# Kernel optimization log

Hardware: AMD Instinct MI355X
Metric: run time of the kernel (lower is better)

The kernel has to match this reference:

```python
import jax, jax.numpy as jnp
import numpy as np

BOS = 1
MAX_LEN = 20


def _lstm_cell(x, h, c, Wih, Whh, bih, bhh):
    # torch.nn.LSTMCell gate order: i, f, g, o
    g = x @ Wih.T + h @ Whh.T + bih + bhh
    i, f, gg, o = jnp.split(g, 4, axis=-1)
    c = jax.nn.sigmoid(f) * c + jax.nn.sigmoid(i) * jnp.tanh(gg)
    h = jax.nn.sigmoid(o) * jnp.tanh(c)
    return h, c


def setup_inputs() -> dict:
    key = jax.random.key(0)
    ks = jax.random.split(key, 12)
    B, K, D = 512, 36, 2048
    A, H, Em, V = 512, 512, 300, 10000
    s = 0.02
    rn = lambda k, shape, sc=s: sc * jax.random.normal(k, shape, dtype=jnp.float32)
    return {
        'feats': jax.random.normal(ks[0], (B, K, D), dtype=jnp.float32),
        'Wp': rn(ks[1], (A, D)), 'bp': jnp.zeros((A,), jnp.float32),
        'E': rn(ks[2], (V, Em), 0.1).at[0].set(0.0),  # padding_idx = 0
        'Wih1': rn(ks[3], (4 * H, Em + A)), 'Whh1': rn(ks[4], (4 * H, H)),
        'bih1': jnp.zeros((4 * H,), jnp.float32), 'bhh1': jnp.zeros((4 * H,), jnp.float32),
        'Wih2': rn(ks[5], (4 * H, H + A)), 'Whh2': rn(ks[6], (4 * H, H)),
        'bih2': jnp.zeros((4 * H,), jnp.float32), 'bhh2': jnp.zeros((4 * H,), jnp.float32),
        'Wa1': rn(ks[7], (A, H + A)), 'ba1': jnp.zeros((A,), jnp.float32),
        'wa2': rn(ks[8], (1, A)), 'ba2': jnp.zeros((1,), jnp.float32),
        'Wo': rn(ks[9], (V, H)), 'bo': jnp.zeros((V,), jnp.float32),
    }


def reference(feats, Wp, bp, E, Wih1, Whh1, bih1, bhh1, Wih2, Whh2, bih2, bhh2,
              Wa1, ba1, wa2, ba2, Wo, bo):
    B, K, D = feats.shape
    H = Whh1.shape[1]
    f_att = feats @ Wp.T + bp                      # [B, K, A]
    f_mean = f_att.mean(axis=1)                    # [B, A]
    # attn Linear over concat([h1, f_att]): split columns, precompute f_att term
    Wa1_h, Wa1_f = Wa1[:, :H], Wa1[:, H:]
    att_f = f_att @ Wa1_f.T + ba1                  # [B, K, A]
    x0 = jnp.broadcast_to(E[BOS], (B, E.shape[1]))
    z = jnp.zeros((B, H), jnp.float32)
    carry0 = (x0, z, z, z, z)

    def step(carry, _):
        x, h1, c1, h2, c2 = carry
        h1, c1 = _lstm_cell(jnp.concatenate([x, f_mean], axis=-1), h1, c1,
                            Wih1, Whh1, bih1, bhh1)
        pre = jnp.tanh(att_f + (h1 @ Wa1_h.T)[:, None, :])   # [B, K, A]
        e = pre @ wa2[0] + ba2[0]                            # [B, K]
        alpha = jax.nn.softmax(e, axis=-1)
        ctx = jnp.einsum('bk,bka->ba', alpha, f_att)         # [B, A]
        h2, c2 = _lstm_cell(jnp.concatenate([h1, ctx], axis=-1), h2, c2,
                            Wih2, Whh2, bih2, bhh2)
        logit = h2 @ Wo.T + bo                               # [B, V]  (dropout is identity in eval)
        nxt = jnp.argmax(logit, axis=-1)
        return (E[nxt], h1, c1, h2, c2), nxt

    _, ids = jax.lax.scan(step, carry0, None, length=MAX_LEN - 1)
    return ids.T  # [B, MAX_LEN-1], matches torch.stack(out_ids, 1)
```

## Files before the change

kernel.cpp:

```cpp
#include <hip/hip_runtime.h>
#include <math.h>
#include <stdint.h>

constexpr int Bsz = 512, Kf = 36, Dd = 2048, Aa = 512, Hh = 512, Em = 300;
constexpr int Vv = 10000, TSTEPS = 19, BOS = 1;
constexpr int K1 = 832;
constexpr int K2 = 1536;
constexpr int VvP = 10112;
constexpr float SPLIT_S  = 2048.0f;
constexpr float SPLIT_IS = 1.0f / 2048.0f;

#define CDIV(a,b) (((a)+(b)-1)/(b))

typedef _Float16 f16x8 __attribute__((ext_vector_type(8)));
typedef float    f32x4 __attribute__((ext_vector_type(4)));

typedef const unsigned int GU __attribute__((address_space(1)));
typedef unsigned int       LU __attribute__((address_space(3)));

__device__ __forceinline__ void gload16(const void* g, void* l) {
    __builtin_amdgcn_global_load_lds((GU*)g, (LU*)l, 16, 0, 0);
}

template<int N> __device__ __forceinline__ void wait_vm() {
    if constexpr (N == 0)       asm volatile("s_waitcnt vmcnt(0)" ::: "memory");
    else if constexpr (N == 4)  asm volatile("s_waitcnt vmcnt(4)" ::: "memory");
    else if constexpr (N == 6)  asm volatile("s_waitcnt vmcnt(6)" ::: "memory");
    else if constexpr (N == 8)  asm volatile("s_waitcnt vmcnt(8)" ::: "memory");
    else static_assert(N == 0, "unsupported vmcnt literal");
}
#define WAIT_LGKM asm volatile("s_waitcnt lgkmcnt(0)" ::: "memory")
#define SB0 __builtin_amdgcn_sched_barrier(0)
#define BAR __builtin_amdgcn_s_barrier()

__device__ __forceinline__ float sigm(float v) { return 1.0f / (1.0f + expf(-v)); }

__device__ __forceinline__ void wsplit(_Float16* __restrict__ hi, _Float16* __restrict__ lo,
                                       size_t idx, float v) {
    _Float16 h = (_Float16)v;
    hi[idx] = h;
    lo[idx] = (_Float16)((v - (float)h) * SPLIT_S);
}

template<int BM, int BN, int BK, bool AF32, bool NFAST, int OCC>
__global__ __launch_bounds__(256, OCC)
void gemm_sp(const float* __restrict__ Af,
             const _Float16* __restrict__ Ahi, const _Float16* __restrict__ Alo, int lda,
             const _Float16* __restrict__ Bhi, const _Float16* __restrict__ Blo, int ldb,
             float* __restrict__ C, int ldc, int N, int K,
             const float* __restrict__ bias1, const float* __restrict__ bias2,
             const float* __restrict__ addC, int gxn)
{
    constexpr int WM = BM / 2, WN = BN / 2;
    constexpr int MF = WM / 16, NF = WN / 16;
    constexpr int PA  = BK / 8;
    constexpr int PSA = BM * 8 + 8;
    constexpr int PSB = BN * 8 + 8;
    constexpr int SZA = PA * PSA, SZB = PA * PSB;
    constexpr int OAH = 0, OAL = SZA, OBH = 2 * SZA, OBL = 2 * SZA + SZB;
    constexpr int BUF = 2 * SZA + 2 * SZB;
    constexpr int NCHA = BM * BK / 2048;
    constexpr int NCHB = BN * BK / 2048;
    constexpr int LW = 2 * NCHA + 2 * NCHB;
    __shared__ _Float16 sm[2 * BUF];

    const int nwg = gridDim.x;
    const int cpx = nwg >> 3;
    const int orig = blockIdx.x;
    const int lid = (orig & 7) * cpx + (orig >> 3);
    int mt, nt;
    if (NFAST) { nt = lid % gxn; mt = lid / gxn; }
    else       { const int gym = nwg / gxn; mt = lid % gym; nt = lid / gym; }
    const int m0 = mt * BM, n0 = nt * BN;

    const int t    = threadIdx.x;
    const int lane = t & 63;
    const int w    = t >> 6;
    const int wr   = w >> 1, wc = w & 1;
    const int l15  = lane & 15, l4 = lane >> 4;

    f32x4 acch[MF][NF];
    f32x4 accm[MF][NF];
    #pragma unroll
    for (int m = 0; m < MF; ++m)
        #pragma unroll
        for (int n = 0; n < NF; ++n) {
            acch[m][n] = (f32x4){0.f, 0.f, 0.f, 0.f};
            accm[m][n] = (f32x4){0.f, 0.f, 0.f, 0.f};
        }

    const int nkt = K / BK;

    auto stageB = [&](int bufo, int kt) {
        #pragma unroll
        for (int i = 0; i < NCHB; ++i) {
            const int q  = i * 256 + t;
            const int p  = q / BN, r = q % BN;
            const int qw = i * 256 + (t & ~63);
            const int pu = qw / BN, ru = qw % BN;
            const size_t goff = (size_t)(n0 + r) * ldb + kt * BK + p * 8;
            gload16(Bhi + goff, &sm[bufo + OBH + pu * PSB + ru * 8]);
            gload16(Blo + goff, &sm[bufo + OBL + pu * PSB + ru * 8]);
        }
    };
    auto stageA16 = [&](int bufo, int kt) {
        #pragma unroll
        for (int i = 0; i < NCHA; ++i) {
            const int q  = i * 256 + t;
            const int p  = q / BM, r = q % BM;
            const int qw = i * 256 + (t & ~63);
            const int pu = qw / BM, ru = qw % BM;
            const size_t goff = (size_t)(m0 + r) * lda + kt * BK + p * 8;
            gload16(Ahi + goff, &sm[bufo + OAH + pu * PSA + ru * 8]);
            gload16(Alo + goff, &sm[bufo + OAL + pu * PSA + ru * 8]);
        }
    };
    auto issueA = [&](float4 (&rd)[NCHA][2], int kt) {
        #pragma unroll
        for (int i = 0; i < NCHA; ++i) {
            const int q = i * 256 + t;
            const int p = q / BM, r = q % BM;
            const float* src = Af + (size_t)(m0 + r) * lda + kt * BK + p * 8;
            rd[i][0] = *(const float4*)src;
            rd[i][1] = *(const float4*)(src + 4);
        }
    };
    auto writeA = [&](int bufo, float4 (&rd)[NCHA][2]) {
        #pragma unroll
        for (int i = 0; i < NCHA; ++i) {
            const int q = i * 256 + t;
            const int p = q / BM, r = q % BM;
            const float f[8] = {rd[i][0].x, rd[i][0].y, rd[i][0].z, rd[i][0].w,
                                rd[i][1].x, rd[i][1].y, rd[i][1].z, rd[i][1].w};
            f16x8 hi, lo;
            #pragma unroll
            for (int j = 0; j < 8; ++j) {
                _Float16 h = (_Float16)f[j];
                hi[j] = h;
                lo[j] = (_Float16)((f[j] - (float)h) * SPLIT_S);
            }
            *(f16x8*)&sm[bufo + OAH + p * PSA + r * 8] = hi;
            *(f16x8*)&sm[bufo + OAL + p * PSA + r * 8] = lo;
        }
    };
    auto compute = [&](int bufo) {
        #pragma unroll
        for (int s = 0; s < BK / 32; ++s) {
            f16x8 ah[MF], al[MF], bh[NF], bl[NF];
            const int pl = s * 4 + l4;
            #pragma unroll
            for (int m = 0; m < MF; ++m) {
                const int row = wr * WM + m * 16 + l15;
                ah[m] = *(const f16x8*)&sm[bufo + OAH + pl * PSA + row * 8];
                al[m] = *(const f16x8*)&sm[bufo + OAL + pl * PSA + row * 8];
            }
            #pragma unroll
            for (int n = 0; n < NF; ++n) {
                const int row = wc * WN + n * 16 + l15;
                bh[n] = *(const f16x8*)&sm[bufo + OBH + pl * PSB + row * 8];
                bl[n] = *(const f16x8*)&sm[bufo + OBL + pl * PSB + row * 8];
            }
            #pragma unroll
            for (int m = 0; m < MF; ++m)
                #pragma unroll
                for (int n = 0; n < NF; ++n) {
                    acch[m][n] = __builtin_amdgcn_mfma_f32_16x16x32_f16(ah[m], bh[n], acch[m][n], 0, 0, 0);
                    accm[m][n] = __builtin_amdgcn_mfma_f32_16x16x32_f16(ah[m], bl[n], accm[m][n], 0, 0, 0);
                    accm[m][n] = __builtin_amdgcn_mfma_f32_16x16x32_f16(al[m], bh[n], accm[m][n], 0, 0, 0);
                }
        }
    };

    if constexpr (AF32) {
        float4 rA[NCHA][2], rB[NCHA][2];
        issueA(rA, 0); stageB(0, 0);
        for (int kt = 0; kt < nkt; kt += 2) {
            issueA(rB, kt + 1); stageB(BUF, kt + 1);
            wait_vm<LW>(); SB0;
            writeA(0, rA);
            WAIT_LGKM; SB0;
            BAR; SB0;
            compute(0);
            SB0; WAIT_LGKM; BAR; SB0;
            if (kt + 2 < nkt) { issueA(rA, kt + 2); stageB(0, kt + 2); wait_vm<LW>(); }
            else              { wait_vm<0>(); }
            SB0;
            writeA(BUF, rB);
            WAIT_LGKM; SB0;
            BAR; SB0;
            compute(BUF);
            SB0; WAIT_LGKM; BAR; SB0;
        }
    } else {
        stageA16(0, 0); stageB(0, 0);
        for (int kt = 0; kt < nkt; ++kt) {
            const int bufc = (kt & 1) ? BUF : 0;
            const int bufn = BUF - bufc;
            if (kt + 1 < nkt) { stageA16(bufn, kt + 1); stageB(bufn, kt + 1); wait_vm<LW>(); }
            else              { wait_vm<0>(); }
            SB0;
            BAR; SB0;
            compute(bufc);
            SB0; WAIT_LGKM; BAR; SB0;
        }
    }

    #pragma unroll
    for (int m = 0; m < MF; ++m) {
        const int rowb = m0 + wr * WM + m * 16 + l4 * 4;
        #pragma unroll
        for (int n = 0; n < NF; ++n) {
            const int col = n0 + wc * WN + n * 16 + l15;
            if (col < N) {
                float bb = 0.f;
                if (bias1) bb += bias1[col];
                if (bias2) bb += bias2[col];
                #pragma unroll
                for (int r = 0; r < 4; ++r) {
                    const size_t idx = (size_t)(rowb + r) * ldc + col;
                    float v = acch[m][n][r] + accm[m][n][r] * SPLIT_IS + bb;
                    if (addC) v += addC[idx];
                    C[idx] = v;
                }
            }
        }
    }
}

__global__ __launch_bounds__(256)
void split_convert(const float* __restrict__ src, int srcld, int validR,
                   _Float16* __restrict__ dhi, _Float16* __restrict__ dlo,
                   int dstld, int coloff, int R, int C)
{
    const int total = R * C;
    for (int i = blockIdx.x * 256 + threadIdx.x; i < total; i += gridDim.x * 256) {
        const int r = i / C, c = i % C;
        const float v = (r < validR) ? src[(size_t)r * srcld + c] : 0.f;
        wsplit(dhi, dlo, (size_t)r * dstld + coloff + c, v);
    }
}

__global__ __launch_bounds__(256)
void transpose_wah(const float* __restrict__ Wa1, float* __restrict__ WahT)
{
    const int i = blockIdx.x * 256 + threadIdx.x;
    if (i < Aa * Hh) {
        const int a = i / Hh, h = i % Hh;
        WahT[(size_t)h * Aa + a] = Wa1[(size_t)a * (Hh + Aa) + h];
    }
}

__global__ __launch_bounds__(256)
void init_kernel(_Float16* __restrict__ a1h, _Float16* __restrict__ a1l,
                 _Float16* __restrict__ a2h, _Float16* __restrict__ a2l,
                 float* __restrict__ c1, float* __restrict__ c2,
                 const float* __restrict__ E)
{
    const int idx = blockIdx.x * 256 + threadIdx.x;
    if (idx < Bsz * K1) {
        const int col = idx % K1;
        const float v = (col < Em) ? E[(size_t)BOS * Em + col] : 0.f;
        wsplit(a1h, a1l, idx, v);
    }
    if (idx < Bsz * K2) wsplit(a2h, a2l, idx, 0.f);
    if (idx < Bsz * Hh) { c1[idx] = 0.f; c2[idx] = 0.f; }
}

__global__ __launch_bounds__(256)
void fmean_kernel(const float* __restrict__ f_att, float* __restrict__ f_mean,
                  _Float16* __restrict__ fmh, _Float16* __restrict__ fml)
{
    const int b = blockIdx.x;
    for (int a = threadIdx.x; a < Aa; a += 256) {
        float s = 0.f;
        for (int k = 0; k < Kf; ++k) s += f_att[((size_t)b * Kf + k) * Aa + a];
        const float v = s * (1.0f / 36.0f);
        f_mean[(size_t)b * Aa + a] = v;
        wsplit(fmh, fml, (size_t)b * Aa + a, v);
    }
}

__global__ __launch_bounds__(256)
void lstm_cell_kernel(const float* __restrict__ g, float* __restrict__ c,
                      _Float16* __restrict__ hhi, _Float16* __restrict__ hlo,
                      int hld, int hoff,
                      _Float16* __restrict__ h2hi, _Float16* __restrict__ h2lo,
                      int h2ld, int h2off)
{
    const int idx = blockIdx.x * 256 + threadIdx.x;
    const int b = idx >> 9, h = idx & 511;
    const float* gb = g + (size_t)b * 2048;
    const float gi = gb[h], gf = gb[512 + h], gc = gb[1024 + h], go = gb[1536 + h];
    const float cv = sigm(gf) * c[idx] + sigm(gi) * tanhf(gc);
    c[idx] = cv;
    const float hv = sigm(go) * tanhf(cv);
    wsplit(hhi, hlo, (size_t)b * hld + hoff + h, hv);
    if (h2hi) wsplit(h2hi, h2lo, (size_t)b * h2ld + h2off + h, hv);
}

__global__ __launch_bounds__(256)
void attn_fused(const float* __restrict__ att_f,
                const _Float16* __restrict__ a2hin, const _Float16* __restrict__ a2lin,
                const float* __restrict__ WahT,
                const float* __restrict__ wa2, const float* __restrict__ ba2,
                const float* __restrict__ f_att,
                _Float16* __restrict__ a2h, _Float16* __restrict__ a2l)
{
    const int b = blockIdx.x, tid = threadIdx.x;
    const int w = tid >> 6, lane = tid & 63;
    __shared__ float sh1[Hh];
    __shared__ float sq[Aa];
    __shared__ float se[Kf];
    __shared__ float wk[Kf];
    for (int h = tid; h < Hh; h += 256)
        sh1[h] = (float)a2hin[(size_t)b * K2 + h] + (float)a2lin[(size_t)b * K2 + h] * SPLIT_IS;
    __syncthreads();
    for (int a = tid; a < Aa; a += 256) {
        float acc = 0.f;
        for (int h = 0; h < Hh; ++h)
            acc = fmaf(sh1[h], WahT[(size_t)h * Aa + a], acc);
        sq[a] = acc;
    }
    __syncthreads();
    for (int k = w; k < Kf; k += 4) {
        const float* pf = att_f + ((size_t)b * Kf + k) * Aa;
        float s = 0.f;
        #pragma unroll
        for (int j = 0; j < Aa; j += 64) {
            const int a = j + lane;
            s += tanhf(pf[a] + sq[a]) * wa2[a];
        }
        #pragma unroll
        for (int off = 32; off; off >>= 1) s += __shfl_down(s, off);
        if (lane == 0) se[k] = s + ba2[0];
    }
    __syncthreads();
    if (tid < Kf) {
        float mx = -INFINITY;
        for (int k = 0; k < Kf; ++k) mx = fmaxf(mx, se[k]);
        float ssum = 0.f;
        for (int k = 0; k < Kf; ++k) ssum += expf(se[k] - mx);
        wk[tid] = expf(se[tid] - mx) / ssum;
    }
    __syncthreads();
    for (int a = tid; a < Aa; a += 256) {
        float acc = 0.f;
        for (int k = 0; k < Kf; ++k)
            acc = fmaf(wk[k], f_att[((size_t)b * Kf + k) * Aa + a], acc);
        wsplit(a2h, a2l, (size_t)b * K2 + Hh + a, acc);
    }
}

__global__ __launch_bounds__(256)
void argmax_embed_kernel(const float* __restrict__ logits, const float* __restrict__ E,
                         _Float16* __restrict__ a1h, _Float16* __restrict__ a1l,
                         int* __restrict__ out, int t)
{
    const int b = blockIdx.x;
    const int tid = threadIdx.x;
    float best = -INFINITY;
    int bi = Vv;
    for (int j = tid; j < Vv; j += 256) {
        const float v = logits[(size_t)b * Vv + j];
        if (v > best) { best = v; bi = j; }
    }
    __shared__ float sv[256];
    __shared__ int   si[256];
    sv[tid] = best; si[tid] = bi;
    __syncthreads();
    for (int s = 128; s > 0; s >>= 1) {
        if (tid < s) {
            const float v2 = sv[tid + s];
            const int   i2 = si[tid + s];
            if (v2 > sv[tid] || (v2 == sv[tid] && i2 < si[tid])) { sv[tid] = v2; si[tid] = i2; }
        }
        __syncthreads();
    }
    const int idx = si[0];
    if (tid == 0) out[(size_t)b * TSTEPS + t] = idx;
    for (int d = tid; d < Em; d += 256)
        wsplit(a1h, a1l, (size_t)b * K1 + d, E[(size_t)idx * Em + d]);
}

static inline void conv(hipStream_t s, const float* src, int srcld, int validR,
                        _Float16* dhi, _Float16* dlo, int dstld, int coloff, int R, int C)
{
    int blocks = CDIV(R * C, 256); if (blocks > 2048) blocks = 2048;
    split_convert<<<dim3(blocks), dim3(256), 0, s>>>(src, srcld, validR, dhi, dlo, dstld, coloff, R, C);
}

extern "C" void kernel_launch(void* const* d_in, const int* in_sizes, int n_in,
                              void* d_out, int out_size, void* d_ws, size_t ws_size,
                              hipStream_t stream)
{
    const float* feats = (const float*)d_in[0];
    const float* Wp    = (const float*)d_in[1];
    const float* bp    = (const float*)d_in[2];
    const float* E     = (const float*)d_in[3];
    const float* Wih1  = (const float*)d_in[4];
    const float* Whh1  = (const float*)d_in[5];
    const float* bih1  = (const float*)d_in[6];
    const float* bhh1  = (const float*)d_in[7];
    const float* Wih2  = (const float*)d_in[8];
    const float* Whh2  = (const float*)d_in[9];
    const float* bih2  = (const float*)d_in[10];
    const float* bhh2  = (const float*)d_in[11];
    const float* Wa1   = (const float*)d_in[12];
    const float* ba1   = (const float*)d_in[13];
    const float* wa2   = (const float*)d_in[14];
    const float* ba2   = (const float*)d_in[15];
    const float* Wo    = (const float*)d_in[16];
    const float* bo    = (const float*)d_in[17];
    int* out = (int*)d_out;
    (void)in_sizes; (void)n_in; (void)out_size; (void)ws_size;

    uint8_t* w = (uint8_t*)d_ws;
    size_t off = 0;
    auto alloc = [&](size_t bytes) { void* p = w + off; off = (off + bytes + 255) & ~(size_t)255; return p; };

    float*     f_att  = (float*)alloc(18432ull * 512 * 4);
    float*     att_f  = (float*)alloc(18432ull * 512 * 4);
    float*     f_mean = (float*)alloc(512ull * 512 * 4);
    _Float16*  fmh    = (_Float16*)alloc(512ull * 512 * 2);
    _Float16*  fml    = (_Float16*)alloc(512ull * 512 * 2);
    _Float16*  wph    = (_Float16*)alloc(512ull * 2048 * 2);
    _Float16*  wpl    = (_Float16*)alloc(512ull * 2048 * 2);
    _Float16*  w1ph   = (_Float16*)alloc(2048ull * K1 * 2);
    _Float16*  w1pl   = (_Float16*)alloc(2048ull * K1 * 2);
    _Float16*  w1ch   = (_Float16*)alloc(2048ull * 512 * 2);
    _Float16*  w1cl   = (_Float16*)alloc(2048ull * 512 * 2);
    _Float16*  w2ph   = (_Float16*)alloc(2048ull * K2 * 2);
    _Float16*  w2pl   = (_Float16*)alloc(2048ull * K2 * 2);
    float*     WahT   = (float*)alloc(512ull * 512 * 4);
    _Float16*  wafh   = (_Float16*)alloc(512ull * 512 * 2);
    _Float16*  wafl   = (_Float16*)alloc(512ull * 512 * 2);
    _Float16*  woh    = (_Float16*)alloc((size_t)VvP * 512 * 2);
    _Float16*  wol    = (_Float16*)alloc((size_t)VvP * 512 * 2);
    float*     g1c    = (float*)alloc(512ull * 2048 * 4);
    _Float16*  a1h    = (_Float16*)alloc(512ull * K1 * 2);
    _Float16*  a1l    = (_Float16*)alloc(512ull * K1 * 2);
    _Float16*  a2h    = (_Float16*)alloc(512ull * K2 * 2);
    _Float16*  a2l    = (_Float16*)alloc(512ull * K2 * 2);
    float*     c1     = (float*)alloc(512ull * 512 * 4);
    float*     c2     = (float*)alloc(512ull * 512 * 4);
    float*     gbuf   = (float*)alloc(512ull * 2048 * 4);
    float*     logits = (float*)alloc(512ull * Vv * 4);

    conv(stream, Wp,          Dd,      512,   wph,  wpl,  2048, 0,    512,  2048);
    conv(stream, Wih1,        Em + Aa, 2048,  w1ph, w1pl, K1,   0,    2048, Em);
    conv(stream, Whh1,        Hh,      2048,  w1ph, w1pl, K1,   Em,   2048, 512);
    conv(stream, Wih1,        Em + Aa, 0,     w1ph, w1pl, K1,   812,  2048, 20);
    conv(stream, Wih1 + Em,   Em + Aa, 2048,  w1ch, w1cl, 512,  0,    2048, 512);
    conv(stream, Wih2,        Hh + Aa, 2048,  w2ph, w2pl, K2,   0,    2048, 1024);
    conv(stream, Whh2,        Hh,      2048,  w2ph, w2pl, K2,   1024, 2048, 512);
    transpose_wah<<<dim3(1024), dim3(256), 0, stream>>>(Wa1, WahT);
    conv(stream, Wa1 + Hh,    Hh + Aa, 512,   wafh, wafl, 512,  0,    512,  512);
    conv(stream, Wo,          Hh,      Vv,    woh,  wol,  512,  0,    VvP,  512);

    init_kernel<<<dim3(CDIV(Bsz * K2, 256)), dim3(256), 0, stream>>>(a1h, a1l, a2h, a2l, c1, c2, E);

    gemm_sp<128, 64, 32, true, true, 2><<<dim3(1152), 256, 0, stream>>>(
        feats, nullptr, nullptr, Dd, wph, wpl, 2048, f_att, 512, 512, 2048, bp, nullptr, nullptr, 8);
    fmean_kernel<<<dim3(Bsz), dim3(256), 0, stream>>>(f_att, f_mean, fmh, fml);
    gemm_sp<64, 64, 32, false, false, 4><<<dim3(256), 256, 0, stream>>>(
        nullptr, fmh, fml, 512, w1ch, w1cl, 512, g1c, 2048, 2048, 512, bih1, bhh1, nullptr, 32);
    gemm_sp<128, 64, 32, true, true, 2><<<dim3(1152), 256, 0, stream>>>(
        f_att, nullptr, nullptr, 512, wafh, wafl, 512, att_f, 512, 512, 512, ba1, nullptr, nullptr, 8);

    for (int t = 0; t < TSTEPS; ++t) {
        gemm_sp<64, 64, 32, false, false, 4><<<dim3(256), 256, 0, stream>>>(
            nullptr, a1h, a1l, K1, w1ph, w1pl, K1, gbuf, 2048, 2048, K1, nullptr, nullptr, g1c, 32);
        lstm_cell_kernel<<<dim3(Bsz * Hh / 256), dim3(256), 0, stream>>>(
            gbuf, c1, a2h, a2l, K2, 0, a1h, a1l, K1, Em);
        attn_fused<<<dim3(Bsz), dim3(256), 0, stream>>>(
            att_f, a2h, a2l, WahT, wa2, ba2, f_att, a2h, a2l);
        gemm_sp<64, 64, 32, false, false, 4><<<dim3(256), 256, 0, stream>>>(
            nullptr, a2h, a2l, K2, w2ph, w2pl, K2, gbuf, 2048, 2048, K2, bih2, bhh2, nullptr, 32);
        lstm_cell_kernel<<<dim3(Bsz * Hh / 256), dim3(256), 0, stream>>>(
            gbuf, c2, a2h, a2l, K2, 1024, nullptr, nullptr, 0, 0);
        gemm_sp<64, 128, 32, false, false, 3><<<dim3(632), 256, 0, stream>>>(
            nullptr, a2h + 1024, a2l + 1024, K2, woh, wol, 512, logits, Vv, Vv, 512, bo, nullptr, nullptr, 79);
        argmax_embed_kernel<<<dim3(Bsz), dim3(256), 0, stream>>>(logits, E, a1h, a1l, out, t);
    }
}
```

Baseline: 3.778 ms.

## Fuse LSTM cell and argmax into GEMM epilogues, triple-buffer fp16 GEMM pipeline

```diff
diff --git a/kernel.cpp b/kernel.cpp
--- a/kernel.cpp
+++ b/kernel.cpp
@@ -7,6 +7,7 @@
 constexpr int K1 = 832;
 constexpr int K2 = 1536;
 constexpr int VvP = 10112;
+constexpr int NTL = VvP / 64;
 constexpr float SPLIT_S  = 2048.0f;
 constexpr float SPLIT_IS = 1.0f / 2048.0f;
 
@@ -27,6 +28,8 @@
     else if constexpr (N == 4)  asm volatile("s_waitcnt vmcnt(4)" ::: "memory");
     else if constexpr (N == 6)  asm volatile("s_waitcnt vmcnt(6)" ::: "memory");
     else if constexpr (N == 8)  asm volatile("s_waitcnt vmcnt(8)" ::: "memory");
+    else if constexpr (N == 12) asm volatile("s_waitcnt vmcnt(12)" ::: "memory");
+    else if constexpr (N == 16) asm volatile("s_waitcnt vmcnt(16)" ::: "memory");
     else static_assert(N == 0, "unsupported vmcnt literal");
 }
 #define WAIT_LGKM asm volatile("s_waitcnt lgkmcnt(0)" ::: "memory")
@@ -42,16 +45,23 @@
     lo[idx] = (_Float16)((v - (float)h) * SPLIT_S);
 }
 
-template<int BM, int BN, int BK, bool AF32, bool NFAST, int OCC>
+
+template<int BM, int BN, int BK, int WVM, bool AF32, bool NFAST, int OCC, int EPI>
 __global__ __launch_bounds__(256, OCC)
 void gemm_sp(const float* __restrict__ Af,
              const _Float16* __restrict__ Ahi, const _Float16* __restrict__ Alo, int lda,
              const _Float16* __restrict__ Bhi, const _Float16* __restrict__ Blo, int ldb,
              float* __restrict__ C, int ldc, int N, int K,
              const float* __restrict__ bias1, const float* __restrict__ bias2,
-             const float* __restrict__ addC, int gxn)
-{
-    constexpr int WM = BM / 2, WN = BN / 2;
+             const float* __restrict__ addC, int gxn,
+             float* __restrict__ cbuf,
+             _Float16* __restrict__ d1h, _Float16* __restrict__ d1l, int ld1, int off1,
+             _Float16* __restrict__ d2h, _Float16* __restrict__ d2l, int ld2, int off2,
+             float* __restrict__ candV, int* __restrict__ candI, int ntl)
+{
+    static_assert(EPI != 2 || WVM == 4, "LSTM epilogue needs 4x1 wave grid");
+    constexpr int WVN = 4 / WVM;
+    constexpr int WM = BM / WVM, WN = BN / WVN;
     constexpr int MF = WM / 16, NF = WN / 16;
     constexpr int PA  = BK / 8;
     constexpr int PSA = BM * 8 + 8;
@@ -62,7 +72,8 @@
     constexpr int NCHA = BM * BK / 2048;
     constexpr int NCHB = BN * BK / 2048;
     constexpr int LW = 2 * NCHA + 2 * NCHB;
-    __shared__ _Float16 sm[2 * BUF];
+    constexpr int NBUF = AF32 ? 2 : 3;
+    __shared__ _Float16 sm[NBUF * BUF];
 
     const int nwg = gridDim.x;
     const int cpx = nwg >> 3;
@@ -76,7 +87,7 @@
     const int t    = threadIdx.x;
     const int lane = t & 63;
     const int w    = t >> 6;
-    const int wr   = w >> 1, wc = w & 1;
+    const int wr   = w / WVN, wc = w % WVN;
     const int l15  = lane & 15, l4 = lane >> 4;
 
     f32x4 acch[MF][NF];
@@ -193,36 +204,127 @@
         }
     } else {
         stageA16(0, 0); stageB(0, 0);
+        stageA16(BUF, 1); stageB(BUF, 1);
         for (int kt = 0; kt < nkt; ++kt) {
-            const int bufc = (kt & 1) ? BUF : 0;
-            const int bufn = BUF - bufc;
-            if (kt + 1 < nkt) { stageA16(bufn, kt + 1); stageB(bufn, kt + 1); wait_vm<LW>(); }
-            else              { wait_vm<0>(); }
+            const int bc = (kt % 3) * BUF;
+            if (kt + 2 < nkt) {
+                stageA16(((kt + 2) % 3) * BUF, kt + 2);
+                stageB(((kt + 2) % 3) * BUF, kt + 2);
+                wait_vm<2 * LW>();
+            } else if (kt + 1 < nkt) {
+                wait_vm<LW>();
+            } else {
+                wait_vm<0>();
+            }
             SB0;
             BAR; SB0;
-            compute(bufc);
+            compute(bc);
             SB0; WAIT_LGKM; BAR; SB0;
         }
     }
 
-    #pragma unroll
-    for (int m = 0; m < MF; ++m) {
-        const int rowb = m0 + wr * WM + m * 16 + l4 * 4;
-        #pragma unroll
-        for (int n = 0; n < NF; ++n) {
-            const int col = n0 + wc * WN + n * 16 + l15;
-            if (col < N) {
+    if constexpr (EPI == 0 || EPI == 1) {
+        #pragma unroll
+        for (int m = 0; m < MF; ++m) {
+            const int rowb = m0 + wr * WM + m * 16 + l4 * 4;
+            #pragma unroll
+            for (int n = 0; n < NF; ++n) {
+                const int col = n0 + wc * WN + n * 16 + l15;
+                if (col < N) {
+                    float bb = 0.f;
+                    if (bias1) {
+                        int bx = col;
+                        if constexpr (EPI == 1)
+                            bx = ((col & 63) >> 4) * 512 + ((col >> 6) << 4) + (col & 15);
+                        bb += bias1[bx];
+                        if (bias2) bb += bias2[bx];
+                    }
+                    #pragma unroll
+                    for (int r = 0; r < 4; ++r) {
+                        const size_t idx = (size_t)(rowb + r) * ldc + col;
+                        float v = acch[m][n][r] + accm[m][n][r] * SPLIT_IS + bb;
+                        if (addC) v += addC[idx];
+                        C[idx] = v;
+                    }
+                }
+            }
+        }
+    } else if constexpr (EPI == 2) {
+        const int hh = (n0 >> 2) + l15;
+        #pragma unroll
+        for (int r = 0; r < 4; ++r) {
+            const int row = m0 + wr * 16 + l4 * 4 + r;
+            float v[4];
+            #pragma unroll
+            for (int n = 0; n < 4; ++n) {
+                const int col = n0 + n * 16 + l15;
                 float bb = 0.f;
-                if (bias1) bb += bias1[col];
-                if (bias2) bb += bias2[col];
+                if (bias1) {
+                    const int bx = ((col & 63) >> 4) * 512 + ((col >> 6) << 4) + (col & 15);
+                    bb = bias1[bx] + bias2[bx];
+                }
+                float x = acch[0][n][r] + accm[0][n][r] * SPLIT_IS + bb;
+                if (addC) x += addC[(size_t)row * ldc + col];
+                v[n] = x;
+            }
+            const float cold = cbuf[(size_t)row * Hh + hh];
+            const float cv = sigm(v[1]) * cold + sigm(v[0]) * tanhf(v[2]);
+            cbuf[(size_t)row * Hh + hh] = cv;
+            const float hv = sigm(v[3]) * tanhf(cv);
+            wsplit(d1h, d1l, (size_t)row * ld1 + off1 + hh, hv);
+            if (d2h) wsplit(d2h, d2l, (size_t)row * ld2 + off2 + hh, hv);
+        }
+    } else {
+        float* sEv = reinterpret_cast<float*>(&sm[0]);
+        int*   sEi = reinterpret_cast<int*>(&sm[0]) + 2 * BM;
+        float bv[MF][4];
+        int   bix[MF][4];
+        #pragma unroll
+        for (int m = 0; m < MF; ++m)
+            #pragma unroll
+            for (int r = 0; r < 4; ++r) { bv[m][r] = -INFINITY; bix[m][r] = 0x7fffffff; }
+        #pragma unroll
+        for (int m = 0; m < MF; ++m)
+            #pragma unroll
+            for (int r = 0; r < 4; ++r)
+                #pragma unroll
+                for (int n = 0; n < NF; ++n) {
+                    const int col = n0 + wc * WN + n * 16 + l15;
+                    if (col < N) {
+                        const float x = acch[m][n][r] + accm[m][n][r] * SPLIT_IS + bias1[col];
+                        if (x > bv[m][r]) { bv[m][r] = x; bix[m][r] = col; }
+                    }
+                }
+        #pragma unroll
+        for (int mask = 1; mask < 16; mask <<= 1) {
+            #pragma unroll
+            for (int m = 0; m < MF; ++m)
                 #pragma unroll
                 for (int r = 0; r < 4; ++r) {
-                    const size_t idx = (size_t)(rowb + r) * ldc + col;
-                    float v = acch[m][n][r] + accm[m][n][r] * SPLIT_IS + bb;
-                    if (addC) v += addC[idx];
-                    C[idx] = v;
+                    const float ov = __shfl_xor(bv[m][r], mask);
+                    const int   oi = __shfl_xor(bix[m][r], mask);
+                    if (ov > bv[m][r] || (ov == bv[m][r] && oi < bix[m][r])) {
+                        bv[m][r] = ov; bix[m][r] = oi;
+                    }
                 }
-            }
+        }
+        if (l15 == 0) {
+            #pragma unroll
+            for (int m = 0; m < MF; ++m)
+                #pragma unroll
+                for (int r = 0; r < 4; ++r) {
+                    const int rl = wr * WM + m * 16 + l4 * 4 + r;
+                    sEv[wc * BM + rl] = bv[m][r];
+                    sEi[wc * BM + rl] = bix[m][r];
+                }
+        }
+        __syncthreads();
+        if (t < BM) {
+            float v0 = sEv[t]; int i0 = sEi[t];
+            const float v1 = sEv[BM + t]; const int i1 = sEi[BM + t];
+            if (v1 > v0 || (v1 == v0 && i1 < i0)) { v0 = v1; i0 = i1; }
+            candV[(size_t)(m0 + t) * ntl + nt] = v0;
+            candI[(size_t)(m0 + t) * ntl + nt] = i0;
         }
     }
 }
@@ -230,13 +332,18 @@
 __global__ __launch_bounds__(256)
 void split_convert(const float* __restrict__ src, int srcld, int validR,
                    _Float16* __restrict__ dhi, _Float16* __restrict__ dlo,
-                   int dstld, int coloff, int R, int C)
+                   int dstld, int coloff, int R, int C, int gperm)
 {
     const int total = R * C;
     for (int i = blockIdx.x * 256 + threadIdx.x; i < total; i += gridDim.x * 256) {
         const int r = i / C, c = i % C;
+        int dr = r;
+        if (gperm) {
+            const int gate = r >> 9, h = r & 511;
+            dr = ((h >> 4) << 6) + (gate << 4) + (h & 15);
+        }
         const float v = (r < validR) ? src[(size_t)r * srcld + c] : 0.f;
-        wsplit(dhi, dlo, (size_t)r * dstld + coloff + c, v);
+        wsplit(dhi, dlo, (size_t)dr * dstld + coloff + c, v);
     }
 }
 
@@ -281,24 +388,6 @@
 }
 
 __global__ __launch_bounds__(256)
-void lstm_cell_kernel(const float* __restrict__ g, float* __restrict__ c,
-                      _Float16* __restrict__ hhi, _Float16* __restrict__ hlo,
-                      int hld, int hoff,
-                      _Float16* __restrict__ h2hi, _Float16* __restrict__ h2lo,
-                      int h2ld, int h2off)
-{
-    const int idx = blockIdx.x * 256 + threadIdx.x;
-    const int b = idx >> 9, h = idx & 511;
-    const float* gb = g + (size_t)b * 2048;
-    const float gi = gb[h], gf = gb[512 + h], gc = gb[1024 + h], go = gb[1536 + h];
-    const float cv = sigm(gf) * c[idx] + sigm(gi) * tanhf(gc);
-    c[idx] = cv;
-    const float hv = sigm(go) * tanhf(cv);
-    wsplit(hhi, hlo, (size_t)b * hld + hoff + h, hv);
-    if (h2hi) wsplit(h2hi, h2lo, (size_t)b * h2ld + h2off + h, hv);
-}
-
-__global__ __launch_bounds__(256)
 void attn_fused(const float* __restrict__ att_f,
                 const _Float16* __restrict__ a2hin, const _Float16* __restrict__ a2lin,
                 const float* __restrict__ WahT,
@@ -306,67 +395,74 @@
                 const float* __restrict__ f_att,
                 _Float16* __restrict__ a2h, _Float16* __restrict__ a2l)
 {
-    const int b = blockIdx.x, tid = threadIdx.x;
+    const int b0 = blockIdx.x * 2, tid = threadIdx.x;
     const int w = tid >> 6, lane = tid & 63;
-    __shared__ float sh1[Hh];
-    __shared__ float sq[Aa];
-    __shared__ float se[Kf];
-    __shared__ float wk[Kf];
-    for (int h = tid; h < Hh; h += 256)
-        sh1[h] = (float)a2hin[(size_t)b * K2 + h] + (float)a2lin[(size_t)b * K2 + h] * SPLIT_IS;
+    __shared__ float sh1[2][Hh];
+    __shared__ float sq[2][Aa];
+    __shared__ float se[2][Kf];
+    __shared__ float wk[2][Kf];
+    for (int i = tid; i < 2 * Hh; i += 256) {
+        const int bb = i >> 9, h = i & 511;
+        sh1[bb][h] = (float)a2hin[(size_t)(b0 + bb) * K2 + h]
+                   + (float)a2lin[(size_t)(b0 + bb) * K2 + h] * SPLIT_IS;
+    }
     __syncthreads();
     for (int a = tid; a < Aa; a += 256) {
-        float acc = 0.f;
-        for (int h = 0; h < Hh; ++h)
-            acc = fmaf(sh1[h], WahT[(size_t)h * Aa + a], acc);
-        sq[a] = acc;
+        float ac0 = 0.f, ac1 = 0.f;
+        for (int h = 0; h < Hh; ++h) {
+            const float wv = WahT[(size_t)h * Aa + a];
+            ac0 = fmaf(sh1[0][h], wv, ac0);
+            ac1 = fmaf(sh1[1][h], wv, ac1);
+        }
+        sq[0][a] = ac0; sq[1][a] = ac1;
     }
     __syncthreads();
-    for (int k = w; k < Kf; k += 4) {
-        const float* pf = att_f + ((size_t)b * Kf + k) * Aa;
+    for (int p = w; p < 2 * Kf; p += 4) {
+        const int bb = p & 1, k = p >> 1;
+        const float* pf = att_f + ((size_t)(b0 + bb) * Kf + k) * Aa;
+        const float* pq = sq[bb];
         float s = 0.f;
         #pragma unroll
         for (int j = 0; j < Aa; j += 64) {
             const int a = j + lane;
-            s += tanhf(pf[a] + sq[a]) * wa2[a];
+            s += tanhf(pf[a] + pq[a]) * wa2[a];
         }
         #pragma unroll
         for (int off = 32; off; off >>= 1) s += __shfl_down(s, off);
-        if (lane == 0) se[k] = s + ba2[0];
+        if (lane == 0) se[bb][k] = s + ba2[0];
     }
     __syncthreads();
-    if (tid < Kf) {
+    if (tid < 2 * Kf) {
+        const int bb = tid / Kf, kk = tid % Kf;
         float mx = -INFINITY;
-        for (int k = 0; k < Kf; ++k) mx = fmaxf(mx, se[k]);
+        for (int k = 0; k < Kf; ++k) mx = fmaxf(mx, se[bb][k]);
         float ssum = 0.f;
-        for (int k = 0; k < Kf; ++k) ssum += expf(se[k] - mx);
-        wk[tid] = expf(se[tid] - mx) / ssum;
+        for (int k = 0; k < Kf; ++k) ssum += expf(se[bb][k] - mx);
+        wk[bb][kk] = expf(se[bb][kk] - mx) / ssum;
     }
     __syncthreads();
-    for (int a = tid; a < Aa; a += 256) {
+    for (int i = tid; i < 2 * Aa; i += 256) {
+        const int bb = i >> 9, a = i & 511;
         float acc = 0.f;
         for (int k = 0; k < Kf; ++k)
-            acc = fmaf(wk[k], f_att[((size_t)b * Kf + k) * Aa + a], acc);
-        wsplit(a2h, a2l, (size_t)b * K2 + Hh + a, acc);
+            acc = fmaf(wk[bb][k], f_att[((size_t)(b0 + bb) * Kf + k) * Aa + a], acc);
+        wsplit(a2h, a2l, (size_t)(b0 + bb) * K2 + Hh + a, acc);
     }
 }
 
 __global__ __launch_bounds__(256)
-void argmax_embed_kernel(const float* __restrict__ logits, const float* __restrict__ E,
+void argmax_embed_kernel(const float* __restrict__ candV, const int* __restrict__ candI,
+                         const float* __restrict__ E,
                          _Float16* __restrict__ a1h, _Float16* __restrict__ a1l,
-                         int* __restrict__ out, int t)
+                         int* __restrict__ out, int t, int ntl)
 {
     const int b = blockIdx.x;
     const int tid = threadIdx.x;
-    float best = -INFINITY;
-    int bi = Vv;
-    for (int j = tid; j < Vv; j += 256) {
-        const float v = logits[(size_t)b * Vv + j];
-        if (v > best) { best = v; bi = j; }
-    }
     __shared__ float sv[256];
     __shared__ int   si[256];
-    sv[tid] = best; si[tid] = bi;
+    float bvv = -INFINITY; int bii = 0x7fffffff;
+    if (tid < ntl) { bvv = candV[(size_t)b * ntl + tid]; bii = candI[(size_t)b * ntl + tid]; }
+    sv[tid] = bvv; si[tid] = bii;
     __syncthreads();
     for (int s = 128; s > 0; s >>= 1) {
         if (tid < s) {
@@ -383,10 +479,12 @@
 }
 
 static inline void conv(hipStream_t s, const float* src, int srcld, int validR,
-                        _Float16* dhi, _Float16* dlo, int dstld, int coloff, int R, int C)
+                        _Float16* dhi, _Float16* dlo, int dstld, int coloff,
+                        int R, int C, int gperm)
 {
     int blocks = CDIV(R * C, 256); if (blocks > 2048) blocks = 2048;
-    split_convert<<<dim3(blocks), dim3(256), 0, s>>>(src, srcld, validR, dhi, dlo, dstld, coloff, R, C);
+    split_convert<<<dim3(blocks), dim3(256), 0, s>>>(src, srcld, validR, dhi, dlo,
+                                                     dstld, coloff, R, C, gperm);
 }
 
 extern "C" void kernel_launch(void* const* d_in, const int* in_sizes, int n_in,
@@ -443,43 +541,52 @@
     _Float16*  a2l    = (_Float16*)alloc(512ull * K2 * 2);
     float*     c1     = (float*)alloc(512ull * 512 * 4);
     float*     c2     = (float*)alloc(512ull * 512 * 4);
-    float*     gbuf   = (float*)alloc(512ull * 2048 * 4);
-    float*     logits = (float*)alloc(512ull * Vv * 4);
-
-    conv(stream, Wp,          Dd,      512,   wph,  wpl,  2048, 0,    512,  2048);
-    conv(stream, Wih1,        Em + Aa, 2048,  w1ph, w1pl, K1,   0,    2048, Em);
-    conv(stream, Whh1,        Hh,      2048,  w1ph, w1pl, K1,   Em,   2048, 512);
-    conv(stream, Wih1,        Em + Aa, 0,     w1ph, w1pl, K1,   812,  2048, 20);
-    conv(stream, Wih1 + Em,   Em + Aa, 2048,  w1ch, w1cl, 512,  0,    2048, 512);
-    conv(stream, Wih2,        Hh + Aa, 2048,  w2ph, w2pl, K2,   0,    2048, 1024);
-    conv(stream, Whh2,        Hh,      2048,  w2ph, w2pl, K2,   1024, 2048, 512);
+    float*     candV  = (float*)alloc(512ull * NTL * 4);
+    int*       candI  = (int*)alloc(512ull * NTL * 4);
+
+    conv(stream, Wp,        Dd,      512,  wph,  wpl,  2048, 0,    512,  2048, 0);
+    conv(stream, Wih1,      Em + Aa, 2048, w1ph, w1pl, K1,   0,    2048, Em,   1);
+    conv(stream, Whh1,      Hh,      2048, w1ph, w1pl, K1,   Em,   2048, 512,  1);
+    conv(stream, Wih1,      Em + Aa, 0,    w1ph, w1pl, K1,   812,  2048, 20,   0);
+    conv(stream, Wih1 + Em, Em + Aa, 2048, w1ch, w1cl, 512,  0,    2048, 512,  1);
+    conv(stream, Wih2,      Hh + Aa, 2048, w2ph, w2pl, K2,   0,    2048, 1024, 1);
+    conv(stream, Whh2,      Hh,      2048, w2ph, w2pl, K2,   1024, 2048, 512,  1);
     transpose_wah<<<dim3(1024), dim3(256), 0, stream>>>(Wa1, WahT);
-    conv(stream, Wa1 + Hh,    Hh + Aa, 512,   wafh, wafl, 512,  0,    512,  512);
-    conv(stream, Wo,          Hh,      Vv,    woh,  wol,  512,  0,    VvP,  512);
+    conv(stream, Wa1 + Hh,  Hh + Aa, 512,  wafh, wafl, 512,  0,    512,  512,  0);
+    conv(stream, Wo,        Hh,      Vv,   woh,  wol,  512,  0,    VvP,  512,  0);
 
     init_kernel<<<dim3(CDIV(Bsz * K2, 256)), dim3(256), 0, stream>>>(a1h, a1l, a2h, a2l, c1, c2, E);
 
-    gemm_sp<128, 64, 32, true, true, 2><<<dim3(1152), 256, 0, stream>>>(
-        feats, nullptr, nullptr, Dd, wph, wpl, 2048, f_att, 512, 512, 2048, bp, nullptr, nullptr, 8);
+    gemm_sp<128, 64, 32, 2, true, true, 2, 0><<<dim3(1152), 256, 0, stream>>>(
+        feats, nullptr, nullptr, Dd, wph, wpl, 2048, f_att, 512, 512, 2048,
+        bp, nullptr, nullptr, 8,
+        nullptr, nullptr, nullptr, 0, 0, nullptr, nullptr, 0, 0, nullptr, nullptr, 0);
     fmean_kernel<<<dim3(Bsz), dim3(256), 0, stream>>>(f_att, f_mean, fmh, fml);
-    gemm_sp<64, 64, 32, false, false, 4><<<dim3(256), 256, 0, stream>>>(
-        nullptr, fmh, fml, 512, w1ch, w1cl, 512, g1c, 2048, 2048, 512, bih1, bhh1, nullptr, 32);
-    gemm_sp<128, 64, 32, true, true, 2><<<dim3(1152), 256, 0, stream>>>(
-        f_att, nullptr, nullptr, 512, wafh, wafl, 512, att_f, 512, 512, 512, ba1, nullptr, nullptr, 8);
+    gemm_sp<64, 64, 32, 2, false, false, 3, 1><<<dim3(256), 256, 0, stream>>>(
+        nullptr, fmh, fml, 512, w1ch, w1cl, 512, g1c, 2048, 2048, 512,
+        bih1, bhh1, nullptr, 32,
+        nullptr, nullptr, nullptr, 0, 0, nullptr, nullptr, 0, 0, nullptr, nullptr, 0);
+    gemm_sp<128, 64, 32, 2, true, true, 2, 0><<<dim3(1152), 256, 0, stream>>>(
+        f_att, nullptr, nullptr, 512, wafh, wafl, 512, att_f, 512, 512, 512,
+        ba1, nullptr, nullptr, 8,
+        nullptr, nullptr, nullptr, 0, 0, nullptr, nullptr, 0, 0, nullptr, nullptr, 0);
 
     for (int t = 0; t < TSTEPS; ++t) {
-        gemm_sp<64, 64, 32, false, false, 4><<<dim3(256), 256, 0, stream>>>(
-            nullptr, a1h, a1l, K1, w1ph, w1pl, K1, gbuf, 2048, 2048, K1, nullptr, nullptr, g1c, 32);
-        lstm_cell_kernel<<<dim3(Bsz * Hh / 256), dim3(256), 0, stream>>>(
-            gbuf, c1, a2h, a2l, K2, 0, a1h, a1l, K1, Em);
-        attn_fused<<<dim3(Bsz), dim3(256), 0, stream>>>(
+        gemm_sp<64, 64, 64, 4, false, false, 1, 2><<<dim3(256), 256, 0, stream>>>(
+            nullptr, a1h, a1l, K1, w1ph, w1pl, K1, nullptr, 2048, 2048, K1,
+            nullptr, nullptr, g1c, 32,
+            c1, a2h, a2l, K2, 0, a1h, a1l, K1, Em, nullptr, nullptr, 0);
+        attn_fused<<<dim3(Bsz / 2), dim3(256), 0, stream>>>(
             att_f, a2h, a2l, WahT, wa2, ba2, f_att, a2h, a2l);
-        gemm_sp<64, 64, 32, false, false, 4><<<dim3(256), 256, 0, stream>>>(
-            nullptr, a2h, a2l, K2, w2ph, w2pl, K2, gbuf, 2048, 2048, K2, bih2, bhh2, nullptr, 32);
-        lstm_cell_kernel<<<dim3(Bsz * Hh / 256), dim3(256), 0, stream>>>(
-            gbuf, c2, a2h, a2l, K2, 1024, nullptr, nullptr, 0, 0);
-        gemm_sp<64, 128, 32, false, false, 3><<<dim3(632), 256, 0, stream>>>(
-            nullptr, a2h + 1024, a2l + 1024, K2, woh, wol, 512, logits, Vv, Vv, 512, bo, nullptr, nullptr, 79);
-        argmax_embed_kernel<<<dim3(Bsz), dim3(256), 0, stream>>>(logits, E, a1h, a1l, out, t);
-    }
-}
+        gemm_sp<64, 64, 64, 4, false, false, 1, 2><<<dim3(256), 256, 0, stream>>>(
+            nullptr, a2h, a2l, K2, w2ph, w2pl, K2, nullptr, 2048, 2048, K2,
+            bih2, bhh2, nullptr, 32,
+            c2, a2h, a2l, K2, 1024, nullptr, nullptr, 0, 0, nullptr, nullptr, 0);
+        gemm_sp<64, 64, 32, 2, false, false, 3, 3><<<dim3(8 * NTL), 256, 0, stream>>>(
+            nullptr, a2h + 1024, a2l + 1024, K2, woh, wol, 512, nullptr, 0, Vv, 512,
+            bo, nullptr, nullptr, NTL,
+            nullptr, nullptr, nullptr, 0, 0, nullptr, nullptr, 0, 0, candV, candI, NTL);
+        argmax_embed_kernel<<<dim3(Bsz), dim3(256), 0, stream>>>(
+            candV, candI, E, a1h, a1l, out, t, NTL);
+    }
+}
```

Result: slower. 4.574 ms (+21.1%).
